# Kernel optimization log

Hardware: AMD Instinct MI355X
Metric: run time of the kernel (lower is better)

The kernel has to match this reference:

```python
import jax, jax.numpy as jnp
import numpy as np

H, D = 8, 32          # num_heads, head dim (hidden = 256)
HID = H * D
LRELU = 0.2
NT, NC, E, FIN = 60000, 30000, 200000, 64


def setup_inputs() -> dict:
    key = jax.random.key(0)
    ks = jax.random.split(key, 24)
    s = 0.05
    inp = {
        'x_trans': jax.random.normal(ks[0], (NT, FIN), jnp.float32),
        'x_cc':    jax.random.normal(ks[1], (NC, FIN), jnp.float32),
        'src_c2t': jax.random.randint(ks[2], (E,), 0, NC),
        'dst_c2t': jax.random.randint(ks[3], (E,), 0, NT),
        'src_t2c': jax.random.randint(ks[4], (E,), 0, NT),
        'dst_t2c': jax.random.randint(ks[5], (E,), 0, NC),
        'W_in': jax.random.normal(ks[6], (2, FIN, HID), jnp.float32) * s,
        'b_in': jnp.zeros((2, HID), jnp.float32),
        'Wk': jax.random.normal(ks[7], (2, 2, HID, HID), jnp.float32) * s,
        'bk': jnp.zeros((2, 2, HID), jnp.float32),
        'Wq': jax.random.normal(ks[8], (2, 2, HID, HID), jnp.float32) * s,
        'bq': jnp.zeros((2, 2, HID), jnp.float32),
        'Wv': jax.random.normal(ks[9], (2, 2, HID, HID), jnp.float32) * s,
        'bv': jnp.zeros((2, 2, HID), jnp.float32),
        'Wa': jax.random.normal(ks[10], (2, 2, HID, HID), jnp.float32) * s,
        'ba': jnp.zeros((2, 2, HID), jnp.float32),
        'a_rel': jax.random.normal(ks[11], (2, 2, H, D, D), jnp.float32) * s,
        'm_rel': jax.random.normal(ks[12], (2, 2, H, D, D), jnp.float32) * s,
        'p_rel': jnp.ones((2, 2, H), jnp.float32),
        'skip':  jnp.ones((2, 2), jnp.float32),
        'W_out': jax.random.normal(ks[13], (HID, 64), jnp.float32) * s,
        'b_out': jnp.zeros((64,), jnp.float32),
    }
    return inp


def _hgt_layer(xs, Wk, bk, Wq, bq, Wv, bv, Wa, ba, a_rel, m_rel, p_rel, skip, edges):
    # xs: list of [N_t, HID] per node type; edges: list of (src_type, dst_type, src_idx, dst_idx)
    nt = len(xs)
    k = [(xs[t] @ Wk[t] + bk[t]).reshape(-1, H, D) for t in range(nt)]
    q = [(xs[t] @ Wq[t] + bq[t]).reshape(-1, H, D) for t in range(nt)]
    v = [(xs[t] @ Wv[t] + bv[t]).reshape(-1, H, D) for t in range(nt)]
    agg = [jnp.zeros((xs[t].shape[0], H, D), xs[t].dtype) for t in range(nt)]
    inv_sqrt_d = 1.0 / jnp.sqrt(jnp.float32(D))
    for r, (st, dt, si, di) in enumerate(edges):
        kr = jnp.einsum('nhd,hde->nhe', k[st], a_rel[r])   # relation-transformed keys
        vr = jnp.einsum('nhd,hde->nhe', v[st], m_rel[r])   # relation-transformed messages
        ke, ve, qe = kr[si], vr[si], q[dt][di]             # [E, H, D] gathers
        alpha = jnp.einsum('ehd,ehd->eh', qe, ke) * p_rel[r] * inv_sqrt_d  # [E, H]
        n_dst = xs[dt].shape[0]
        m = jax.ops.segment_max(alpha, di, num_segments=n_dst)
        ex = jnp.exp(alpha - m[di])
        ssum = jax.ops.segment_sum(ex, di, num_segments=n_dst)
        w = ex / (ssum[di] + 1e-16)                         # segment softmax per dst node
        agg[dt] = agg[dt] + jax.ops.segment_sum(ve * w[..., None], di, num_segments=n_dst)
    out = []
    for t in range(nt):
        o = jax.nn.gelu(agg[t].reshape(-1, HID), approximate=False)
        o = o @ Wa[t] + ba[t]
        beta = jax.nn.sigmoid(skip[t])
        out.append(beta * o + (1.0 - beta) * xs[t])
    return out


def reference(x_trans, x_cc, src_c2t, dst_c2t, src_t2c, dst_t2c,
              W_in, b_in, Wk, bk, Wq, bq, Wv, bv, Wa, ba,
              a_rel, m_rel, p_rel, skip, W_out, b_out):
    # per-node-type Linear + in-place relu
    xs = [jax.nn.relu(x_trans @ W_in[0] + b_in[0]),
          jax.nn.relu(x_cc @ W_in[1] + b_in[1])]
    # relation 0: cc_node -> trans_node ; relation 1: trans_node -> cc_node
    edges = [(1, 0, src_c2t, dst_c2t), (0, 1, src_t2c, dst_t2c)]
    n_layers = Wk.shape[0]
    for l in range(n_layers):
        xs = _hgt_layer(xs, Wk[l], bk[l], Wq[l], bq[l], Wv[l], bv[l], Wa[l], ba[l],
                        a_rel[l], m_rel[l], p_rel[l], skip[l], edges)
    # dropout is identity in eval mode
    y = xs[0] @ W_out + b_out
    y = jnp.where(y > 0, y, LRELU * y)                      # LeakyReLU(0.2)
    n = jnp.linalg.norm(y, axis=1, keepdims=True)
    return y / jnp.maximum(n, 1e-12)                        # F.normalize(p=2, dim=1)
```

## Files before the change

### kernel.cpp

```cpp
#include <hip/hip_runtime.h>
#include <hip/hip_bf16.h>
#include <math.h>

#define NTN 60000
#define NCN 30000
#define NED 200000

typedef unsigned short u16;
typedef unsigned long long u64;
typedef __attribute__((ext_vector_type(8))) u16 u16x8;
typedef __attribute__((ext_vector_type(8))) __bf16 bf16x8;
typedef __attribute__((ext_vector_type(4))) float f32x4;

static __device__ __forceinline__ float bf2f(u16 u) {
    return __uint_as_float(((unsigned)u) << 16);
}
static __device__ __forceinline__ u16 f2bf(float f) {
    unsigned u = __float_as_uint(f);
    unsigned r = (u + 0x7fffu + ((u >> 16) & 1u)) >> 16;
    return (u16)r;
}

__global__ void fill2(unsigned* __restrict__ a, int na, unsigned* __restrict__ b, int nb) {
    int i = blockIdx.x * blockDim.x + threadIdx.x;
    int st = gridDim.x * blockDim.x;
    for (int k = i; k < na; k += st) a[k] = 0u;
    for (int k = i; k < nb; k += st) b[k] = 0u;
}

__global__ void f32_to_bf16_2(const float* __restrict__ in0, u16* __restrict__ out0, int n40,
                              const float* __restrict__ in1, u16* __restrict__ out1, int n41) {
    int i = blockIdx.x * blockDim.x + threadIdx.x;
    int stride = gridDim.x * blockDim.x;
    for (int k = i; k < n40; k += stride) {
        float4 v = ((const float4*)in0)[k];
        ushort4 o;
        o.x = f2bf(v.x); o.y = f2bf(v.y); o.z = f2bf(v.z); o.w = f2bf(v.w);
        ((ushort4*)out0)[k] = o;
    }
    for (int k = i; k < n41; k += stride) {
        float4 v = ((const float4*)in1)[k];
        ushort4 o;
        o.x = f2bf(v.x); o.y = f2bf(v.y); o.z = f2bf(v.z); o.w = f2bf(v.w);
        ((ushort4*)out1)[k] = o;
    }
}

__global__ void convTb(const float* __restrict__ in, u16* __restrict__ out,
                       int K, int N, int inStride, int outStride, int nm) {
    int idx = blockIdx.x * blockDim.x + threadIdx.x;
    int per = N * (K >> 2);
    int total = per * nm;
    if (idx >= total) return;
    int mat = idx / per, rem = idx - mat * per;
    int k4 = rem / N, n = rem - k4 * N;
    int k = k4 * 4;
    const float* src = in + (size_t)mat * inStride;
    u16* dst = out + (size_t)mat * outStride;
    ushort4 o;
    o.x = f2bf(src[(size_t)(k + 0) * N + n]);
    o.y = f2bf(src[(size_t)(k + 1) * N + n]);
    o.z = f2bf(src[(size_t)(k + 2) * N + n]);
    o.w = f2bf(src[(size_t)(k + 3) * N + n]);
    *(ushort4*)(dst + (size_t)n * K + k) = o;
}

__global__ void convT4(const float* __restrict__ s0, u16* __restrict__ d0, int is0, int os0,
                       const float* __restrict__ s1, u16* __restrict__ d1, int is1, int os1,
                       const float* __restrict__ s2, u16* __restrict__ d2, int is2, int os2,
                       const float* __restrict__ s3, u16* __restrict__ d3, int is3, int os3) {
    const float* in; u16* out; int inStride, outStride;
    switch (blockIdx.y) {
        case 0: in = s0; out = d0; inStride = is0; outStride = os0; break;
        case 1: in = s1; out = d1; inStride = is1; outStride = os1; break;
        case 2: in = s2; out = d2; inStride = is2; outStride = os2; break;
        default: in = s3; out = d3; inStride = is3; outStride = os3; break;
    }
    int idx = blockIdx.x * blockDim.x + threadIdx.x;
    const int per = 256 * 64;
    int mat = idx / per, rem = idx - mat * per;
    int k4 = rem >> 8, n = rem & 255;
    int k = k4 * 4;
    const float* src = in + (size_t)mat * inStride;
    u16* dst = out + (size_t)mat * outStride;
    ushort4 o;
    o.x = f2bf(src[(size_t)(k + 0) * 256 + n]);
    o.y = f2bf(src[(size_t)(k + 1) * 256 + n]);
    o.z = f2bf(src[(size_t)(k + 2) * 256 + n]);
    o.w = f2bf(src[(size_t)(k + 3) * 256 + n]);
    *(ushort4*)(dst + (size_t)n * 256 + k) = o;
}

__global__ void copy_bq(const float* __restrict__ bq, float* __restrict__ bqkv) {
    int lt = blockIdx.x;
    bqkv[lt * 768 + threadIdx.x] = bq[lt * 256 + threadIdx.x];
}

__global__ __launch_bounds__(256) void fuse_weights(
    const float* __restrict__ Wk, const float* __restrict__ bk,
    const float* __restrict__ Wv, const float* __restrict__ bv,
    const float* __restrict__ a_rel, const float* __restrict__ m_rel,
    const float* __restrict__ p_rel,
    float* __restrict__ Wf2, float* __restrict__ bqkv)
{
    __shared__ float kw[256], vw[256];
    const int c = blockIdx.x, lt = blockIdx.y, tid = threadIdx.x;
    const int l = lt >> 1, t = lt & 1;
    const int lr = l * 2 + (t == 1 ? 0 : 1);
    const float* WkP = Wk + (size_t)lt * 65536;
    const float* WvP = Wv + (size_t)lt * 65536;
    const float* ar = a_rel + (size_t)lr * 8192;
    const float* mr = m_rel + (size_t)lr * 8192;
    kw[tid] = WkP[c * 256 + tid];
    vw[tid] = WvP[c * 256 + tid];
    __syncthreads();
    const int h = tid >> 5, e = tid & 31;
    const float s = p_rel[lr * 8 + h] * 0.17677669529663687f;
    float ak = 0.f, av = 0.f;
#pragma unroll 8
    for (int d = 0; d < 32; ++d) {
        ak += kw[h * 32 + d] * ar[h * 1024 + d * 32 + e];
        av += vw[h * 32 + d] * mr[h * 1024 + d * 32 + e];
    }
    float* WkfP = Wf2 + (size_t)lt * 131072;
    WkfP[c * 256 + tid] = ak * s;
    WkfP[65536 + c * 256 + tid] = av;
    if (c == 0) {
        const float* bkP = bk + (size_t)lt * 256;
        const float* bvP = bv + (size_t)lt * 256;
        float bka = 0.f, bva = 0.f;
#pragma unroll 8
        for (int d = 0; d < 32; ++d) {
            bka += bkP[h * 32 + d] * ar[h * 1024 + d * 32 + e];
            bva += bvP[h * 32 + d] * mr[h * 1024 + d * 32 + e];
        }
        bqkv[lt * 768 + 256 + tid] = bka * s;
        bqkv[lt * 768 + 512 + tid] = bva;
    }
}

template <int EPI, int BN, bool OBF, int KT>
__global__ __launch_bounds__(256) void gemm_mfma2(
    int nblk0,
    const u16* __restrict__ A0, const u16* __restrict__ W0, const float* __restrict__ b0,
    void* __restrict__ C0, int M0, int ldC0, int NY0,
    const u16* __restrict__ xr0, const float* __restrict__ sk0,
    const u16* __restrict__ A1, const u16* __restrict__ W1, const float* __restrict__ b1,
    void* __restrict__ C1, int M1, int ldC1, int NY1,
    const u16* __restrict__ xr1, const float* __restrict__ sk1)
{
    constexpr int ASZ = 64 * 64;
    constexpr int BSZ = BN * 64;
    constexpr int NF = BN / 32;
    constexpr int NT = KT >> 6;
    constexpr int L = 2 + NF;
    __shared__ u16 smem[3 * (ASZ + BSZ)];

    const int nwg = gridDim.x;
    const int bid = blockIdx.x;
    const int q8 = nwg >> 3, r8 = nwg & 7;
    const int xcd = bid & 7, pos = bid >> 3;
    const int lbid = (xcd < r8) ? xcd * (q8 + 1) + pos
                                : r8 * (q8 + 1) + (xcd - r8) * q8 + pos;

    const u16* A; const u16* WT; const float* bias; void* Cv;
    int M, ldC, NY, sb; const u16* xres; const float* skipPtr;
    if (lbid < nblk0) {
        A = A0; WT = W0; bias = b0; Cv = C0; M = M0; ldC = ldC0; NY = NY0;
        xres = xr0; skipPtr = sk0; sb = lbid;
    } else {
        A = A1; WT = W1; bias = b1; Cv = C1; M = M1; ldC = ldC1; NY = NY1;
        xres = xr1; skipPtr = sk1; sb = lbid - nblk0;
    }
    const int bx = sb / NY, by = sb - bx * NY;
    const int m0 = bx * 64, n0 = by * BN;

    const int tid = threadIdx.x;
    const int wave = tid >> 6, lane = tid & 63;
    const int wm = (wave >> 1) * 32, wn = (wave & 1) * (BN / 2);
    f32x4 acc[2][NF];
#pragma unroll
    for (int i = 0; i < 2; ++i)
#pragma unroll
        for (int j = 0; j < NF; ++j) acc[i][j] = (f32x4){0.f, 0.f, 0.f, 0.f};

    const int sr = lane >> 3;
    const int sl = lane & 7;

    const u16* gpa[2];
    const u16* gpb[NF];
#pragma unroll
    for (int i = 0; i < 2; ++i) {
        int r = wave * 16 + i * 8 + sr;
        int gr = m0 + r; gr = gr < M ? gr : M - 1;
        gpa[i] = A + (size_t)gr * KT + ((sl ^ sr) << 3);
    }
#pragma unroll
    for (int i = 0; i < NF; ++i) {
        int r = wave * (BN / 4) + i * 8 + sr;
        gpb[i] = WT + (size_t)(n0 + r) * KT + ((sl ^ sr) << 3);
    }

    auto stage = [&](int t, int buf) {
        const int k0 = t << 6;
        u16* Ad = smem + buf * (ASZ + BSZ);
        u16* Bd = Ad + ASZ;
#pragma unroll
        for (int i = 0; i < 2; ++i) {
            int rb = wave * 16 + i * 8;
            __builtin_amdgcn_global_load_lds(
                (const __attribute__((address_space(1))) void*)(gpa[i] + k0),
                (__attribute__((address_space(3))) void*)(Ad + rb * 64), 16, 0, 0);
        }
#pragma unroll
        for (int i = 0; i < NF; ++i) {
            int rb = wave * (BN / 4) + i * 8;
            __builtin_amdgcn_global_load_lds(
                (const __attribute__((address_space(1))) void*)(gpb[i] + k0),
                (__attribute__((address_space(3))) void*)(Bd + rb * 64), 16, 0, 0);
        }
    };

    auto compute = [&](int buf) {
        const u16* Ab = smem + buf * (ASZ + BSZ);
        const u16* Bb = Ab + ASZ;
#pragma unroll
        for (int kx = 0; kx < 2; ++kx) {
            bf16x8 af[2], bfr[NF];
#pragma unroll
            for (int mf = 0; mf < 2; ++mf) {
                int r = wm + mf * 16 + (lane & 15);
                int slot = (lane >> 4) + kx * 4;
                af[mf] = __builtin_bit_cast(bf16x8,
                    *(const u16x8*)(Ab + r * 64 + ((slot ^ (r & 7)) << 3)));
            }
#pragma unroll
            for (int nf = 0; nf < NF; ++nf) {
                int r = wn + nf * 16 + (lane & 15);
                int slot = (lane >> 4) + kx * 4;
                bfr[nf] = __builtin_bit_cast(bf16x8,
                    *(const u16x8*)(Bb + r * 64 + ((slot ^ (r & 7)) << 3)));
            }
#pragma unroll
            for (int mf = 0; mf < 2; ++mf)
#pragma unroll
                for (int nf = 0; nf < NF; ++nf)
                    acc[mf][nf] = __builtin_amdgcn_mfma_f32_16x16x32_bf16(
                        af[mf], bfr[nf], acc[mf][nf], 0, 0, 0);
        }
    };

    stage(0, 0);
    if constexpr (NT >= 2) stage(1, 1);
#pragma unroll
    for (int t = 0; t < NT; ++t) {
        if (t + 2 < NT) {
            stage(t + 2, (t + 2) % 3);
            __builtin_amdgcn_sched_barrier(0);
        }
        const int rem = NT - 1 - t;
        const int wc = (rem >= 2) ? 2 * L : rem * L;
        if (wc == 0)       asm volatile("s_waitcnt vmcnt(0)" ::: "memory");
        else if (wc == 4)  asm volatile("s_waitcnt vmcnt(4)" ::: "memory");
        else if (wc == 6)  asm volatile("s_waitcnt vmcnt(6)" ::: "memory");
        else if (wc == 8)  asm volatile("s_waitcnt vmcnt(8)" ::: "memory");
        else               asm volatile("s_waitcnt vmcnt(12)" ::: "memory");
        __builtin_amdgcn_s_barrier();
        __builtin_amdgcn_sched_barrier(0);
        compute(t % 3);
        __builtin_amdgcn_sched_barrier(0);
        __builtin_amdgcn_s_barrier();
        __builtin_amdgcn_sched_barrier(0);
    }

    float beta = 0.f;
    if (EPI == 2) beta = 1.f / (1.f + expf(-skipPtr[0]));

    if constexpr (OBF) {
        constexpr int CLD = BN + 12;
        u16* Ct = smem;
#pragma unroll
        for (int nf = 0; nf < NF; ++nf) {
            int col = wn + nf * 16 + (lane & 15);
            int gcol = n0 + col;
            float bs = bias[gcol];
#pragma unroll
            for (int mf = 0; mf < 2; ++mf) {
#pragma unroll
                for (int j = 0; j < 4; ++j) {
                    int row = wm + mf * 16 + (lane >> 4) * 4 + j;
                    int grow = m0 + row;
                    int gr2 = grow < M ? grow : 0;
                    float c = acc[mf][nf][j] + bs;
                    if (EPI == 1) c = fmaxf(c, 0.f);
                    if (EPI == 2) c = beta * c + (1.f - beta) * bf2f(xres[(size_t)gr2 * ldC + gcol]);
                    if (EPI == 3) c = (c > 0.f) ? c : 0.2f * c;
                    Ct[row * CLD + col] = f2bf(c);
                }
            }
        }
        __syncthreads();
        int row = tid >> 2, c0 = (tid & 3) * (BN / 4);
        int grow = m0 + row;
        if (grow < M) {
            u16* dst = (u16*)Cv + (size_t)grow * ldC + n0 + c0;
            const u16* src = Ct + row * CLD + c0;
#pragma unroll
            for (int i = 0; i < BN / 32; ++i)
                *(u16x8*)(dst + i * 8) = *(const u16x8*)(src + i * 8);
        }
    } else {
#pragma unroll
        for (int nf = 0; nf < NF; ++nf) {
            int gcol = n0 + wn + nf * 16 + (lane & 15);
            float bs = bias[gcol];
#pragma unroll
            for (int mf = 0; mf < 2; ++mf) {
#pragma unroll
                for (int j = 0; j < 4; ++j) {
                    int grow = m0 + wm + mf * 16 + (lane >> 4) * 4 + j;
                    if (grow >= M) continue;
                    float c = acc[mf][nf][j] + bs;
                    if (EPI == 1) c = fmaxf(c, 0.f);
                    if (EPI == 3) c = (c > 0.f) ? c : 0.2f * c;
                    ((float*)Cv)[(size_t)grow * ldC + gcol] = c;
                }
            }
        }
    }
}

__global__ void hist2(const int* __restrict__ d0, unsigned* __restrict__ c0,
                      const int* __restrict__ d1, unsigned* __restrict__ c1, int E) {
    int e = blockIdx.x * blockDim.x + threadIdx.x;
    if (e < E) {
        atomicAdd(&c0[d0[e]], 1u);
        atomicAdd(&c1[d1[e]], 1u);
    }
}

__global__ __launch_bounds__(256) void scan_blocks2(
    const unsigned* __restrict__ c0, unsigned* __restrict__ p0, unsigned* __restrict__ bs0, int N0,
    const unsigned* __restrict__ c1, unsigned* __restrict__ p1, unsigned* __restrict__ bs1, int N1)
{
    const unsigned* counts = blockIdx.y ? c1 : c0;
    unsigned* pref = blockIdx.y ? p1 : p0;
    unsigned* bsum = blockIdx.y ? bs1 : bs0;
    int N = blockIdx.y ? N1 : N0;
    if ((int)blockIdx.x * 256 >= N) return;
    __shared__ unsigned tmp[256];
    int i = blockIdx.x * 256 + threadIdx.x;
    unsigned v = (i < N) ? counts[i] : 0u;
    tmp[threadIdx.x] = v;
    __syncthreads();
    for (int off = 1; off < 256; off <<= 1) {
        unsigned t = (threadIdx.x >= off) ? tmp[threadIdx.x - off] : 0u;
        __syncthreads();
        tmp[threadIdx.x] += t;
        __syncthreads();
    }
    if (i < N) pref[i] = tmp[threadIdx.x] - v;
    if (threadIdx.x == 255) bsum[blockIdx.x] = tmp[255];
}

__global__ __launch_bounds__(256) void scan_top2(
    unsigned* __restrict__ bs0, int NB0, unsigned* __restrict__ bs1, int NB1)
{
    unsigned* bsum = blockIdx.x ? bs1 : bs0;
    int NB = blockIdx.x ? NB1 : NB0;
    __shared__ unsigned tmp[256];
    unsigned v = ((int)threadIdx.x < NB) ? bsum[threadIdx.x] : 0u;
    tmp[threadIdx.x] = v;
    __syncthreads();
    for (int off = 1; off < 256; off <<= 1) {
        unsigned t = (threadIdx.x >= off) ? tmp[threadIdx.x - off] : 0u;
        __syncthreads();
        tmp[threadIdx.x] += t;
        __syncthreads();
    }
    if ((int)threadIdx.x < NB) bsum[threadIdx.x] = tmp[threadIdx.x] - v;
}

__global__ void scan_add2(
    const unsigned* __restrict__ p0, const unsigned* __restrict__ bs0,
    const unsigned* __restrict__ c0, unsigned* __restrict__ cur0, u64* __restrict__ ri0, int N0,
    const unsigned* __restrict__ p1, const unsigned* __restrict__ bs1,
    const unsigned* __restrict__ c1, unsigned* __restrict__ cur1, u64* __restrict__ ri1, int N1)
{
    const unsigned* pref = blockIdx.y ? p1 : p0;
    const unsigned* bsum = blockIdx.y ? bs1 : bs0;
    const unsigned* counts = blockIdx.y ? c1 : c0;
    unsigned* cursor = blockIdx.y ? cur1 : cur0;
    u64* rowinfo = blockIdx.y ? ri1 : ri0;
    int N = blockIdx.y ? N1 : N0;
    int i = blockIdx.x * 256 + threadIdx.x;
    if (i < N) {
        unsigned s = pref[i] + bsum[blockIdx.x];
        cursor[i] = s;
        rowinfo[i] = (u64)s | ((u64)counts[i] << 32);
    }
}

__global__ void place2(const int* __restrict__ d0, const int* __restrict__ s0,
                       unsigned* __restrict__ cur0, unsigned* __restrict__ o0,
                       const int* __restrict__ d1, const int* __restrict__ s1,
                       unsigned* __restrict__ cur1, unsigned* __restrict__ o1, int E) {
    int e = blockIdx.x * blockDim.x + threadIdx.x;
    if (e < E) {
        unsigned p = atomicAdd(&cur0[d0[e]], 1u);
        o0[p] = (unsigned)s0[e] * 768u;
        unsigned q = atomicAdd(&cur1[d1[e]], 1u);
        o1[q] = (unsigned)s1[e] * 768u;
    }
}

#define TBLK8 ((NTN + 7) / 8)
__global__ __launch_bounds__(256) void edge_gather2(
    const u16* __restrict__ qkvT, const u16* __restrict__ qkvC,
    const u64* __restrict__ riT, const unsigned* __restrict__ srcT,
    const u64* __restrict__ riC, const unsigned* __restrict__ srcC,
    u16* __restrict__ aggT, u16* __restrict__ aggC)
{
    const int b = blockIdx.x;
    const bool isT = b < TBLK8;
    const int lane = threadIdx.x & 63;
    const int lq = lane & 31;
    const int n = (((isT ? b : b - TBLK8) << 2) + (int)(threadIdx.x >> 6)) * 2 + (lane >> 5);

    const u16* qkv_d = isT ? qkvT : qkvC;
    const u16* qkv_s = isT ? qkvC : qkvT;
    const u64* ri = isT ? riT : riC;
    const unsigned* srcarr = isT ? srcT : srcC;
    u16* agg = isT ? aggT : aggC;

    const u64 rinfo = ri[n];
    const unsigned start = (unsigned)rinfo;
    const unsigned deg = (unsigned)(rinfo >> 32);
    u16* outp = &agg[(size_t)n * 256 + lq * 8];

    if (deg == 0) {
        *(u16x8*)outp = (u16x8){0, 0, 0, 0, 0, 0, 0, 0};
        return;
    }

    u16x8 qv = *(const u16x8*)&qkv_d[(size_t)n * 768 + lq * 8];
    float qf[8];
#pragma unroll
    for (int i = 0; i < 8; ++i) qf[i] = bf2f(qv[i]);

    const u16* kvb = qkv_s + 256 + lq * 8;
    float m = -INFINITY, s = 0.f;
    float acc[8] = {0.f, 0.f, 0.f, 0.f, 0.f, 0.f, 0.f, 0.f};

    unsigned off = srcarr[start];
    u16x8 kr = *(const u16x8*)(kvb + off);
    u16x8 vr = *(const u16x8*)(kvb + off + 256);
    for (unsigned j = 0;;) {
        const bool more = (j + 1 < deg);
        u16x8 kr_n, vr_n;
        if (more) {
            unsigned off2 = srcarr[start + j + 1];
            kr_n = *(const u16x8*)(kvb + off2);
            vr_n = *(const u16x8*)(kvb + off2 + 256);
        }
        float kf[8];
#pragma unroll
        for (int i = 0; i < 8; ++i) kf[i] = bf2f(kr[i]);
        float p = qf[0] * kf[0] + qf[1] * kf[1] + qf[2] * kf[2] + qf[3] * kf[3]
                + qf[4] * kf[4] + qf[5] * kf[5] + qf[6] * kf[6] + qf[7] * kf[7];
        p += __shfl_xor(p, 1);
        p += __shfl_xor(p, 2);
        float vf[8];
#pragma unroll
        for (int i = 0; i < 8; ++i) vf[i] = bf2f(vr[i]);
        if (__ballot(p > m) == 0ull) {
            float wv = __expf(p - m);
            s += wv;
#pragma unroll
            for (int i = 0; i < 8; ++i) acc[i] += wv * vf[i];
        } else {
            float mn = fmaxf(m, p);
            float sc = __expf(m - mn);
            float wv = __expf(p - mn);
            s = s * sc + wv;
#pragma unroll
            for (int i = 0; i < 8; ++i) acc[i] = acc[i] * sc + wv * vf[i];
            m = mn;
        }
        if (!more) break;
        kr = kr_n; vr = vr_n; ++j;
    }

    float inv = 1.f / (s + 1e-16f);
    u16x8 ov;
#pragma unroll
    for (int i = 0; i < 8; ++i) {
        float x = acc[i] * inv;
        float y2 = 1.5957691216f * x + 0.0713548163f * x * x * x;
        float e = __expf(y2);
        float t = 1.f - 2.f / (e + 1.f);
        ov[i] = f2bf(0.5f * x * (1.f + t));
    }
    *(u16x8*)outp = ov;
}

__global__ __launch_bounds__(256) void norm_rows(float* __restrict__ y, int M) {
    int row = blockIdx.x * 4 + (threadIdx.x >> 6);
    int lane = threadIdx.x & 63;
    if (row >= M) return;
    float v = y[(size_t)row * 64 + lane];
    float s = v * v;
#pragma unroll
    for (int off = 1; off < 64; off <<= 1) s += __shfl_xor(s, off);
    float n = sqrtf(s);
    y[(size_t)row * 64 + lane] = v / fmaxf(n, 1e-12f);
}

extern "C" void kernel_launch(void* const* d_in, const int* in_sizes, int n_in,
                              void* d_out, int out_size, void* d_ws, size_t ws_size,
                              hipStream_t stream)
{
    const float* x_trans = (const float*)d_in[0];
    const float* x_cc    = (const float*)d_in[1];
    const int* src_c2t   = (const int*)d_in[2];
    const int* dst_c2t   = (const int*)d_in[3];
    const int* src_t2c   = (const int*)d_in[4];
    const int* dst_t2c   = (const int*)d_in[5];
    const float* W_in = (const float*)d_in[6];
    const float* b_in = (const float*)d_in[7];
    const float* Wk   = (const float*)d_in[8];
    const float* bk   = (const float*)d_in[9];
    const float* Wq   = (const float*)d_in[10];
    const float* bq   = (const float*)d_in[11];
    const float* Wv   = (const float*)d_in[12];
    const float* bv   = (const float*)d_in[13];
    const float* Wa   = (const float*)d_in[14];
    const float* ba   = (const float*)d_in[15];
    const float* a_rel = (const float*)d_in[16];
    const float* m_rel = (const float*)d_in[17];
    const float* p_rel = (const float*)d_in[18];
    const float* skip  = (const float*)d_in[19];
    const float* W_out = (const float*)d_in[20];
    const float* b_out = (const float*)d_in[21];

    char* w = (char*)d_ws;
    auto alloc = [&](size_t bytes) { char* p = w; w += (bytes + 255) & ~(size_t)255; return p; };
    u16* xs0  = (u16*)alloc((size_t)NTN * 256 * 2);
    u16* xs1  = (u16*)alloc((size_t)NCN * 256 * 2);
    u16* xin0 = (u16*)alloc((size_t)NTN * 64 * 2);
    u16* xin1 = (u16*)alloc((size_t)NCN * 64 * 2);
    u16* qkv0 = (u16*)alloc((size_t)NTN * 768 * 2);
    u16* qkv1 = (u16*)alloc((size_t)NCN * 768 * 2);
    u16* agg0 = (u16*)alloc((size_t)NTN * 256 * 2);
    u16* agg1 = (u16*)alloc((size_t)NCN * 256 * 2);
    u16* WinT = (u16*)alloc((size_t)2 * 16384 * 2);
    u16* WqkvT= (u16*)alloc((size_t)4 * 196608 * 2);
    u16* WaT  = (u16*)alloc((size_t)4 * 65536 * 2);
    u16* WoutT= (u16*)alloc((size_t)16384 * 2);
    float* Wf2 = (float*)alloc((size_t)4 * 131072 * 4);
    float* bqkv = (float*)alloc((size_t)4 * 768 * 4);
    unsigned* countsT   = (unsigned*)alloc((size_t)NTN * 4);
    unsigned* prefT     = (unsigned*)alloc((size_t)NTN * 4);
    unsigned* cursorT   = (unsigned*)alloc((size_t)NTN * 4);
    u64* rowinfoT       = (u64*)alloc((size_t)NTN * 8);
    unsigned* srcAT     = (unsigned*)alloc((size_t)NED * 4);
    unsigned* countsC   = (unsigned*)alloc((size_t)NCN * 4);
    unsigned* prefC     = (unsigned*)alloc((size_t)NCN * 4);
    unsigned* cursorC   = (unsigned*)alloc((size_t)NCN * 4);
    u64* rowinfoC       = (u64*)alloc((size_t)NCN * 8);
    unsigned* srcAC     = (unsigned*)alloc((size_t)NED * 4);
    unsigned* bsum      = (unsigned*)alloc((size_t)2 * 256 * 4);
    (void)ws_size; (void)in_sizes; (void)n_in; (void)out_size;

    {
        const int EB = (NED + 255) / 256;
        const int NBt = (NTN + 255) / 256, NBc = (NCN + 255) / 256;
        fill2<<<256, 256, 0, stream>>>(countsT, NTN, countsC, NCN);
        hist2<<<EB, 256, 0, stream>>>(dst_c2t, countsT, dst_t2c, countsC, NED);
        scan_blocks2<<<dim3(NBt, 2), 256, 0, stream>>>(countsT, prefT, bsum, NTN,
                                                       countsC, prefC, bsum + 256, NCN);
        scan_top2<<<2, 256, 0, stream>>>(bsum, NBt, bsum + 256, NBc);
        scan_add2<<<dim3(NBt, 2), 256, 0, stream>>>(
            prefT, bsum, countsT, cursorT, rowinfoT, NTN,
            prefC, bsum + 256, countsC, cursorC, rowinfoC, NCN);
        place2<<<EB, 256, 0, stream>>>(dst_c2t, src_c2t, cursorT, srcAT,
                                       dst_t2c, src_t2c, cursorC, srcAC, NED);
    }

    fuse_weights<<<dim3(256, 4), 256, 0, stream>>>(Wk, bk, Wv, bv, a_rel, m_rel, p_rel, Wf2, bqkv);
    copy_bq<<<4, 256, 0, stream>>>(bq, bqkv);
    convT4<<<dim3(256, 4), 256, 0, stream>>>(
        Wq, WqkvT, 65536, 196608,
        Wf2, WqkvT + 65536, 131072, 196608,
        Wf2 + 65536, WqkvT + 131072, 131072, 196608,
        Wa, WaT, 65536, 65536);
    convTb<<<(2 * 4096 + 255) / 256, 256, 0, stream>>>(W_in, WinT, 64, 256, 16384, 16384, 2);
    convTb<<<(4096 + 255) / 256, 256, 0, stream>>>(W_out, WoutT, 256, 64, 16384, 16384, 1);
    f32_to_bf16_2<<<1024, 256, 0, stream>>>(x_trans, xin0, NTN * 64 / 4,
                                            x_cc, xin1, NCN * 64 / 4);

    const int GT = (NTN + 63) / 64, GC = (NCN + 63) / 64;

    gemm_mfma2<1, 64, true, 64><<<GT * 4 + GC * 4, 256, 0, stream>>>(
        GT * 4,
        xin0, WinT, b_in, xs0, NTN, 256, 4, nullptr, nullptr,
        xin1, WinT + 16384, b_in + 256, xs1, NCN, 256, 4, nullptr, nullptr);

    for (int l = 0; l < 2; ++l) {
        size_t lt0 = (size_t)(l * 2 + 0), lt1 = (size_t)(l * 2 + 1);

        gemm_mfma2<0, 64, true, 256><<<GT * 12 + GC * 12, 256, 0, stream>>>(
            GT * 12,
            xs0, WqkvT + lt0 * 196608, bqkv + lt0 * 768, qkv0, NTN, 768, 12, nullptr, nullptr,
            xs1, WqkvT + lt1 * 196608, bqkv + lt1 * 768, qkv1, NCN, 768, 12, nullptr, nullptr);

        edge_gather2<<<TBLK8 + (NCN + 7) / 8, 256, 0, stream>>>(
            qkv0, qkv1,
            rowinfoT, srcAT,
            rowinfoC, srcAC,
            agg0, agg1);

        gemm_mfma2<2, 64, true, 256><<<GT * 4 + GC * 4, 256, 0, stream>>>(
            GT * 4,
            agg0, WaT + lt0 * 65536, ba + lt0 * 256, xs0, NTN, 256, 4, xs0, skip + l * 2 + 0,
            agg1, WaT + lt1 * 65536, ba + lt1 * 256, xs1, NCN, 256, 4, xs1, skip + l * 2 + 1);
    }

    {
        float* y = (float*)d_out;
        gemm_mfma2<3, 64, false, 256><<<GT, 256, 0, stream>>>(
            GT,
            xs0, WoutT, b_out, y, NTN, 64, 1, nullptr, nullptr,
            xs0, WoutT, b_out, y, NTN, 64, 1, nullptr, nullptr);
        norm_rows<<<NTN / 4, 256, 0, stream>>>(y, NTN);
    }
}
```

Before: 485.5 us.

## Restructure GEMM into wave-private tiles with B operands loaded straight to registers

Replaces the block-cooperative 64x64 GEMM tile with a 128x64 block where each wave owns a private 32-row A slice in its own LDS region and loads B fragments from global memory directly into registers. This drops the block-wide s_barrier pairs per K step and the shared B staging. The intent is to cut synchronisation overhead and LDS traffic. In exchange, B is re-fetched by every wave (more global/L2 traffic), register pressure rises from the double-buffered B registers, and the A pipeline drops from triple to double buffering.

```diff
diff --git a/kernel.cpp b/kernel.cpp
--- a/kernel.cpp
+++ b/kernel.cpp
@@ -139,8 +139,8 @@
     }
 }
 
-template <int EPI, int BN, bool OBF, int KT>
-__global__ __launch_bounds__(256) void gemm_mfma2(
+template <int EPI, bool OBF, int KT>
+__global__ __launch_bounds__(256) void gemm_wp(
     int nblk0,
     const u16* __restrict__ A0, const u16* __restrict__ W0, const float* __restrict__ b0,
     void* __restrict__ C0, int M0, int ldC0, int NY0,
@@ -149,12 +149,8 @@
     void* __restrict__ C1, int M1, int ldC1, int NY1,
     const u16* __restrict__ xr1, const float* __restrict__ sk1)
 {
-    constexpr int ASZ = 64 * 64;
-    constexpr int BSZ = BN * 64;
-    constexpr int NF = BN / 32;
     constexpr int NT = KT >> 6;
-    constexpr int L = 2 + NF;
-    __shared__ u16 smem[3 * (ASZ + BSZ)];
+    __shared__ u16 smem[16384];
 
     const int nwg = gridDim.x;
     const int bid = blockIdx.x;
@@ -173,122 +169,102 @@
         xres = xr1; skipPtr = sk1; sb = lbid - nblk0;
     }
     const int bx = sb / NY, by = sb - bx * NY;
-    const int m0 = bx * 64, n0 = by * BN;
-
     const int tid = threadIdx.x;
     const int wave = tid >> 6, lane = tid & 63;
-    const int wm = (wave >> 1) * 32, wn = (wave & 1) * (BN / 2);
-    f32x4 acc[2][NF];
-#pragma unroll
-    for (int i = 0; i < 2; ++i)
-#pragma unroll
-        for (int j = 0; j < NF; ++j) acc[i][j] = (f32x4){0.f, 0.f, 0.f, 0.f};
+    const int m0 = bx * 128 + wave * 32;
+    const int n0 = by * 64;
+
+    u16* Ab0 = smem + wave * 4096;
+    u16* Ab1 = Ab0 + 2048;
 
     const int sr = lane >> 3;
     const int sl = lane & 7;
 
-    const u16* gpa[2];
-    const u16* gpb[NF];
-#pragma unroll
-    for (int i = 0; i < 2; ++i) {
-        int r = wave * 16 + i * 8 + sr;
-        int gr = m0 + r; gr = gr < M ? gr : M - 1;
+    const u16* gpa[4];
+#pragma unroll
+    for (int i = 0; i < 4; ++i) {
+        int gr = m0 + i * 8 + sr; gr = gr < M ? gr : M - 1;
         gpa[i] = A + (size_t)gr * KT + ((sl ^ sr) << 3);
     }
-#pragma unroll
-    for (int i = 0; i < NF; ++i) {
-        int r = wave * (BN / 4) + i * 8 + sr;
-        gpb[i] = WT + (size_t)(n0 + r) * KT + ((sl ^ sr) << 3);
-    }
-
-    auto stage = [&](int t, int buf) {
-        const int k0 = t << 6;
-        u16* Ad = smem + buf * (ASZ + BSZ);
-        u16* Bd = Ad + ASZ;
-#pragma unroll
-        for (int i = 0; i < 2; ++i) {
-            int rb = wave * 16 + i * 8;
+    const u16* gpb[4];
+#pragma unroll
+    for (int i = 0; i < 4; ++i)
+        gpb[i] = WT + (size_t)(n0 + i * 16 + (lane & 15)) * KT + ((lane >> 4) << 3);
+
+    f32x4 acc[2][4];
+#pragma unroll
+    for (int i = 0; i < 2; ++i)
+#pragma unroll
+        for (int j = 0; j < 4; ++j) acc[i][j] = (f32x4){0.f, 0.f, 0.f, 0.f};
+
+    u16x8 Breg[2][4][2];
+
+    auto stageA = [&](int t, u16* dst) {
+#pragma unroll
+        for (int i = 0; i < 4; ++i)
             __builtin_amdgcn_global_load_lds(
-                (const __attribute__((address_space(1))) void*)(gpa[i] + k0),
-                (__attribute__((address_space(3))) void*)(Ad + rb * 64), 16, 0, 0);
-        }
-#pragma unroll
-        for (int i = 0; i < NF; ++i) {
-            int rb = wave * (BN / 4) + i * 8;
-            __builtin_amdgcn_global_load_lds(
-                (const __attribute__((address_space(1))) void*)(gpb[i] + k0),
-                (__attribute__((address_space(3))) void*)(Bd + rb * 64), 16, 0, 0);
-        }
+                (const __attribute__((address_space(1))) void*)(gpa[i] + t * 64),
+                (__attribute__((address_space(3))) void*)(dst + i * 512), 16, 0, 0);
     };
-
-    auto compute = [&](int buf) {
-        const u16* Ab = smem + buf * (ASZ + BSZ);
-        const u16* Bb = Ab + ASZ;
-#pragma unroll
-        for (int kx = 0; kx < 2; ++kx) {
-            bf16x8 af[2], bfr[NF];
-#pragma unroll
-            for (int mf = 0; mf < 2; ++mf) {
-                int r = wm + mf * 16 + (lane & 15);
+    auto loadB = [&](int t, int s) {
+#pragma unroll
+        for (int nf = 0; nf < 4; ++nf)
+#pragma unroll
+            for (int kx = 0; kx < 2; ++kx)
+                Breg[s][nf][kx] = *(const u16x8*)(gpb[nf] + t * 64 + kx * 32);
+    };
+
+    stageA(0, Ab0); loadB(0, 0);
+    if constexpr (NT >= 2) { stageA(1, Ab1); loadB(1, 1); }
+
+#pragma unroll
+    for (int t = 0; t < NT; ++t) {
+        const int pb = t & 1;
+        if (t + 1 < NT) asm volatile("s_waitcnt vmcnt(12)" ::: "memory");
+        else            asm volatile("s_waitcnt vmcnt(0)" ::: "memory");
+        __builtin_amdgcn_sched_barrier(0);
+        const u16* Ab = pb ? Ab1 : Ab0;
+        bf16x8 af[2][2];
+#pragma unroll
+        for (int mf = 0; mf < 2; ++mf)
+#pragma unroll
+            for (int kx = 0; kx < 2; ++kx) {
+                int r = mf * 16 + (lane & 15);
                 int slot = (lane >> 4) + kx * 4;
-                af[mf] = __builtin_bit_cast(bf16x8,
+                af[mf][kx] = __builtin_bit_cast(bf16x8,
                     *(const u16x8*)(Ab + r * 64 + ((slot ^ (r & 7)) << 3)));
             }
-#pragma unroll
-            for (int nf = 0; nf < NF; ++nf) {
-                int r = wn + nf * 16 + (lane & 15);
-                int slot = (lane >> 4) + kx * 4;
-                bfr[nf] = __builtin_bit_cast(bf16x8,
-                    *(const u16x8*)(Bb + r * 64 + ((slot ^ (r & 7)) << 3)));
-            }
+        asm volatile("s_waitcnt lgkmcnt(0)" ::: "memory");
+        __builtin_amdgcn_sched_barrier(0);
+        if (t + 2 < NT) stageA(t + 2, pb ? Ab1 : Ab0);
+#pragma unroll
+        for (int kx = 0; kx < 2; ++kx)
 #pragma unroll
             for (int mf = 0; mf < 2; ++mf)
 #pragma unroll
-                for (int nf = 0; nf < NF; ++nf)
+                for (int nf = 0; nf < 4; ++nf)
                     acc[mf][nf] = __builtin_amdgcn_mfma_f32_16x16x32_bf16(
-                        af[mf], bfr[nf], acc[mf][nf], 0, 0, 0);
-        }
-    };
-
-    stage(0, 0);
-    if constexpr (NT >= 2) stage(1, 1);
-#pragma unroll
-    for (int t = 0; t < NT; ++t) {
-        if (t + 2 < NT) {
-            stage(t + 2, (t + 2) % 3);
-            __builtin_amdgcn_sched_barrier(0);
-        }
-        const int rem = NT - 1 - t;
-        const int wc = (rem >= 2) ? 2 * L : rem * L;
-        if (wc == 0)       asm volatile("s_waitcnt vmcnt(0)" ::: "memory");
-        else if (wc == 4)  asm volatile("s_waitcnt vmcnt(4)" ::: "memory");
-        else if (wc == 6)  asm volatile("s_waitcnt vmcnt(6)" ::: "memory");
-        else if (wc == 8)  asm volatile("s_waitcnt vmcnt(8)" ::: "memory");
-        else               asm volatile("s_waitcnt vmcnt(12)" ::: "memory");
-        __builtin_amdgcn_s_barrier();
-        __builtin_amdgcn_sched_barrier(0);
-        compute(t % 3);
-        __builtin_amdgcn_sched_barrier(0);
-        __builtin_amdgcn_s_barrier();
-        __builtin_amdgcn_sched_barrier(0);
+                        af[mf][kx], __builtin_bit_cast(bf16x8, Breg[pb][nf][kx]),
+                        acc[mf][nf], 0, 0, 0);
+        if (t + 2 < NT) loadB(t + 2, pb);
     }
 
     float beta = 0.f;
     if (EPI == 2) beta = 1.f / (1.f + expf(-skipPtr[0]));
 
     if constexpr (OBF) {
-        constexpr int CLD = BN + 12;
-        u16* Ct = smem;
-#pragma unroll
-        for (int nf = 0; nf < NF; ++nf) {
-            int col = wn + nf * 16 + (lane & 15);
+        constexpr int CLD = 68;
+        u16* Ct = smem + wave * 4096;
+#pragma unroll
+        for (int nf = 0; nf < 4; ++nf) {
+            int col = nf * 16 + (lane & 15);
             int gcol = n0 + col;
             float bs = bias[gcol];
 #pragma unroll
             for (int mf = 0; mf < 2; ++mf) {
 #pragma unroll
                 for (int j = 0; j < 4; ++j) {
-                    int row = wm + mf * 16 + (lane >> 4) * 4 + j;
+                    int row = mf * 16 + (lane >> 4) * 4 + j;
                     int grow = m0 + row;
                     int gr2 = grow < M ? grow : 0;
                     float c = acc[mf][nf][j] + bs;
@@ -299,26 +275,25 @@
                 }
             }
         }
-        __syncthreads();
-        int row = tid >> 2, c0 = (tid & 3) * (BN / 4);
+        int row = lane >> 1, c0 = (lane & 1) * 32;
         int grow = m0 + row;
         if (grow < M) {
             u16* dst = (u16*)Cv + (size_t)grow * ldC + n0 + c0;
             const u16* src = Ct + row * CLD + c0;
 #pragma unroll
-            for (int i = 0; i < BN / 32; ++i)
+            for (int i = 0; i < 4; ++i)
                 *(u16x8*)(dst + i * 8) = *(const u16x8*)(src + i * 8);
         }
     } else {
 #pragma unroll
-        for (int nf = 0; nf < NF; ++nf) {
-            int gcol = n0 + wn + nf * 16 + (lane & 15);
+        for (int nf = 0; nf < 4; ++nf) {
+            int gcol = n0 + nf * 16 + (lane & 15);
             float bs = bias[gcol];
 #pragma unroll
             for (int mf = 0; mf < 2; ++mf) {
 #pragma unroll
                 for (int j = 0; j < 4; ++j) {
-                    int grow = m0 + wm + mf * 16 + (lane >> 4) * 4 + j;
+                    int grow = m0 + mf * 16 + (lane >> 4) * 4 + j;
                     if (grow >= M) continue;
                     float c = acc[mf][nf][j] + bs;
                     if (EPI == 1) c = fmaxf(c, 0.f);
@@ -599,9 +574,9 @@
     f32_to_bf16_2<<<1024, 256, 0, stream>>>(x_trans, xin0, NTN * 64 / 4,
                                             x_cc, xin1, NCN * 64 / 4);
 
-    const int GT = (NTN + 63) / 64, GC = (NCN + 63) / 64;
-
-    gemm_mfma2<1, 64, true, 64><<<GT * 4 + GC * 4, 256, 0, stream>>>(
+    const int GT = (NTN + 127) / 128, GC = (NCN + 127) / 128;
+
+    gemm_wp<1, true, 64><<<GT * 4 + GC * 4, 256, 0, stream>>>(
         GT * 4,
         xin0, WinT, b_in, xs0, NTN, 256, 4, nullptr, nullptr,
         xin1, WinT + 16384, b_in + 256, xs1, NCN, 256, 4, nullptr, nullptr);
@@ -609,7 +584,7 @@
     for (int l = 0; l < 2; ++l) {
         size_t lt0 = (size_t)(l * 2 + 0), lt1 = (size_t)(l * 2 + 1);
 
-        gemm_mfma2<0, 64, true, 256><<<GT * 12 + GC * 12, 256, 0, stream>>>(
+        gemm_wp<0, true, 256><<<GT * 12 + GC * 12, 256, 0, stream>>>(
             GT * 12,
             xs0, WqkvT + lt0 * 196608, bqkv + lt0 * 768, qkv0, NTN, 768, 12, nullptr, nullptr,
             xs1, WqkvT + lt1 * 196608, bqkv + lt1 * 768, qkv1, NCN, 768, 12, nullptr, nullptr);
@@ -620,7 +595,7 @@
             rowinfoC, srcAC,
             agg0, agg1);
 
-        gemm_mfma2<2, 64, true, 256><<<GT * 4 + GC * 4, 256, 0, stream>>>(
+        gemm_wp<2, true, 256><<<GT * 4 + GC * 4, 256, 0, stream>>>(
             GT * 4,
             agg0, WaT + lt0 * 65536, ba + lt0 * 256, xs0, NTN, 256, 4, xs0, skip + l * 2 + 0,
             agg1, WaT + lt1 * 65536, ba + lt1 * 256, xs1, NCN, 256, 4, xs1, skip + l * 2 + 1);
@@ -628,7 +603,7 @@
 
     {
         float* y = (float*)d_out;
-        gemm_mfma2<3, 64, false, 256><<<GT, 256, 0, stream>>>(
+        gemm_wp<3, false, 256><<<GT, 256, 0, stream>>>(
             GT,
             xs0, WoutT, b_out, y, NTN, 64, 1, nullptr, nullptr,
             xs0, WoutT, b_out, y, NTN, 64, 1, nullptr, nullptr);
```

Measured after the change: 705.0 us. 45.2% more time.
